# Kernel optimization log

Hardware: AMD Instinct MI355X
Metric: run time of the kernel (lower is better)

## Reference

```python
import jax, jax.numpy as jnp
import numpy as np

B, S, DIM, H = 1, 4096, 1024, 16
HEAD_DIM = DIM // H
ROPE_THETA = 10000.0
LN_EPS = 1e-5


def _rope_cos_sin(seq_len, dim, theta):
    # frequencies over the FULL model dim (rope applied before head split, as in source)
    inv_freq = 1.0 / (theta ** (jnp.arange(0, dim, 2, dtype=jnp.float32) / dim))  # (dim/2,)
    ang = jnp.arange(seq_len, dtype=jnp.float32)[:, None] * inv_freq[None, :]     # (S, dim/2)
    cos = jnp.concatenate([jnp.cos(ang), jnp.cos(ang)], axis=-1)                  # (S, dim)
    sin = jnp.concatenate([jnp.sin(ang), jnp.sin(ang)], axis=-1)
    return cos, sin


def _rotate_half(x):
    d = x.shape[-1] // 2
    return jnp.concatenate([-x[..., d:], x[..., :d]], axis=-1)


def _apply_rope(x, cos, sin):
    # x: (B, S, dim); cos/sin: (S, dim)
    return x * cos[None] + _rotate_half(x) * sin[None]


def setup_inputs() -> dict:
    key = jax.random.key(0)
    ks = jax.random.split(key, 5)
    sc = 1.0 / np.sqrt(DIM)
    return {
        "x": jax.random.normal(ks[0], (B, S, DIM), dtype=jnp.float32),
        "Wqkv": jax.random.normal(ks[1], (DIM, 3 * DIM), dtype=jnp.float32) * sc,
        "bqkv": jax.random.normal(ks[2], (3 * DIM,), dtype=jnp.float32) * 0.01,
        "Wo": jax.random.normal(ks[3], (DIM, DIM), dtype=jnp.float32) * sc,
        "bo": jax.random.normal(ks[4], (DIM,), dtype=jnp.float32) * 0.01,
        "gamma": jnp.ones((DIM,), dtype=jnp.float32),
        "beta": jnp.zeros((DIM,), dtype=jnp.float32),
    }


def reference(x, Wqkv, bqkv, Wo, bo, gamma, beta):
    b, s, d = x.shape
    qkv = x @ Wqkv + bqkv                      # (B, S, 3*dim)
    q, k, v = jnp.split(qkv, 3, axis=-1)       # each (B, S, dim)
    cos, sin = _rope_cos_sin(s, d, ROPE_THETA)
    q = _apply_rope(q, cos, sin)
    k = _apply_rope(k, cos, sin)
    # split heads
    q = q.reshape(b, s, H, HEAD_DIM)
    k = k.reshape(b, s, H, HEAD_DIM)
    v = v.reshape(b, s, H, HEAD_DIM)
    scale = 1.0 / np.sqrt(HEAD_DIM)
    scores = jnp.einsum('bqhd,bkhd->bhqk', q, k) * scale  # (B, H, S, S)
    causal = jnp.triu(jnp.ones((s, s), dtype=bool), k=1)
    scores = jnp.where(causal[None, None], -jnp.inf, scores)
    attn = jax.nn.softmax(scores, axis=-1)
    out = jnp.einsum('bhqk,bkhd->bqhd', attn, v).reshape(b, s, d)
    out = out @ Wo + bo
    # LayerNorm (dropout is identity in eval mode)
    mu = jnp.mean(out, axis=-1, keepdims=True)
    var = jnp.mean(jnp.square(out - mu), axis=-1, keepdims=True)
    return (out - mu) * jax.lax.rsqrt(var + LN_EPS) * gamma + beta
```

## Files before the change

kernel.cpp:

```cpp
#include <hip/hip_runtime.h>
#include <cstdint>
#include <cstddef>

#define S_LEN 4096
#define DIM   1024
#define NH    16
#define HD    64
#define QKV_N 3072

typedef __attribute__((ext_vector_type(8))) short short8;
typedef __attribute__((ext_vector_type(4))) float f32x4;
typedef __attribute__((ext_vector_type(4))) unsigned short ushort4v;
typedef __attribute__((ext_vector_type(2))) unsigned int uint2v;

__device__ inline unsigned short f2bf(float x) {
    unsigned int u = __builtin_bit_cast(unsigned int, x);
    u += 0x7fffu + ((u >> 16) & 1u);
    return (unsigned short)(u >> 16);
}
__device__ inline float bf2f(unsigned short u) {
    return __builtin_bit_cast(float, (unsigned int)u << 16);
}
__device__ inline unsigned int pack2_bf16_rh(float lo, float hi) {
    unsigned int a = __builtin_bit_cast(unsigned int, lo) + 0x8000u;
    unsigned int b = __builtin_bit_cast(unsigned int, hi) + 0x8000u;
    return __builtin_amdgcn_perm(b, a, 0x07060302u);
}

__device__ inline void gl_lds16(const void* g, void* l) {
    __builtin_amdgcn_global_load_lds(
        (const __attribute__((address_space(1))) void*)g,
        (__attribute__((address_space(3))) void*)l, 16, 0, 0);
}

template <bool BF16OUT>
__global__ __launch_bounds__(256) void gemm_mfma_kernel(
    const unsigned short* __restrict__ A,
    const unsigned short* __restrict__ Bt,
    const float* __restrict__ bias,
    void* __restrict__ Cv,
    int M, int N, int K)
{
    __shared__ unsigned short As[128 * 32];
    __shared__ unsigned short Bs[128 * 32];

    const int t    = threadIdx.x;
    const int w    = t >> 6;
    const int lane = t & 63;
    const int ln   = lane & 15;
    const int quad = lane >> 4;
    const int bm   = blockIdx.y * 128;
    const int bn   = blockIdx.x * 128;
    const int wm   = (w & 1) * 64;
    const int wn   = (w >> 1) * 64;

    f32x4 acc[4][4];
#pragma unroll
    for (int i = 0; i < 4; ++i)
#pragma unroll
        for (int j = 0; j < 4; ++j) acc[i][j] = (f32x4){0.f, 0.f, 0.f, 0.f};

    const int lr = lane >> 2;
    const int lc = (lane & 3) * 8;
    const unsigned short* ga = A  + (size_t)(bm + w * 32 + lr) * K + lc;
    const unsigned short* gb = Bt + (size_t)(bn + w * 32 + lr) * K + lc;
    unsigned short* la = &As[(w * 32) * 32];
    unsigned short* lb = &Bs[(w * 32) * 32];

    for (int k0 = 0; k0 < K; k0 += 32) {
        gl_lds16(ga,            la);
        gl_lds16(ga + 16 * K,   la + 16 * 32);
        gl_lds16(gb,            lb);
        gl_lds16(gb + 16 * K,   lb + 16 * 32);
        ga += 32; gb += 32;
        __syncthreads();

        short8 af[4], bf[4];
#pragma unroll
        for (int i = 0; i < 4; ++i)
            af[i] = *(const short8*)&As[(wm + i * 16 + ln) * 32 + quad * 8];
#pragma unroll
        for (int j = 0; j < 4; ++j)
            bf[j] = *(const short8*)&Bs[(wn + j * 16 + ln) * 32 + quad * 8];
#pragma unroll
        for (int i = 0; i < 4; ++i)
#pragma unroll
            for (int j = 0; j < 4; ++j)
                acc[i][j] = __builtin_amdgcn_mfma_f32_16x16x32_bf16(af[i], bf[j], acc[i][j], 0, 0, 0);
        __syncthreads();
    }

#pragma unroll
    for (int j = 0; j < 4; ++j) {
        const int col = bn + wn + j * 16 + ln;
        const float bv = bias[col];
#pragma unroll
        for (int i = 0; i < 4; ++i) {
            const int row0 = bm + wm + i * 16 + quad * 4;
#pragma unroll
            for (int r = 0; r < 4; ++r) {
                const float v = acc[i][j][r] + bv;
                if (BF16OUT)
                    ((unsigned short*)Cv)[(size_t)(row0 + r) * N + col] = f2bf(v);
                else
                    ((float*)Cv)[(size_t)(row0 + r) * N + col] = v;
            }
        }
    }
}

__global__ __launch_bounds__(256) void prep1_kernel(
    const float* __restrict__ x, unsigned short* __restrict__ xb,
    const float* __restrict__ Wqkv, unsigned short* __restrict__ WqkvT,
    const float* __restrict__ Wo, unsigned short* __restrict__ WoT)
{
    __shared__ unsigned short L[64][72];
    const int b = blockIdx.x;
    const int t = threadIdx.x;

    if (b < 2048) {
        const size_t i = ((size_t)b * 256 + t) * 8;
        float4 a = *(const float4*)(x + i);
        float4 c = *(const float4*)(x + i + 4);
        short8 p = { (short)f2bf(a.x), (short)f2bf(a.y), (short)f2bf(a.z), (short)f2bf(a.w),
                     (short)f2bf(c.x), (short)f2bf(c.y), (short)f2bf(c.z), (short)f2bf(c.w) };
        *(short8*)(xb + i) = p;
        return;
    }
    const float* W;
    unsigned short* Wt;
    int N, n0, k0;
    if (b < 2816) {
        const int wb = b - 2048;
        W = Wqkv; Wt = WqkvT; N = QKV_N;
        n0 = (wb % 48) * 64; k0 = (wb / 48) * 64;
    } else {
        const int wb = b - 2816;
        W = Wo; Wt = WoT; N = DIM;
        n0 = (wb & 15) * 64; k0 = (wb >> 4) * 64;
    }
    const int kr = t >> 2, cb = (t & 3) * 16;
    const float* wp = W + (size_t)(k0 + kr) * N + n0 + cb;
#pragma unroll
    for (int u = 0; u < 16; u += 4) {
        float4 v = *(const float4*)(wp + u);
        ushort4v p = { f2bf(v.x), f2bf(v.y), f2bf(v.z), f2bf(v.w) };
        *(ushort4v*)&L[kr][cb + u] = p;
    }
    __syncthreads();
    const int nr = t >> 2, kb = (t & 3) * 16;
    short8 lo, hi;
#pragma unroll
    for (int u = 0; u < 8; ++u) lo[u] = (short)L[kb + u][nr];
#pragma unroll
    for (int u = 0; u < 8; ++u) hi[u] = (short)L[kb + 8 + u][nr];
    unsigned short* op = Wt + (size_t)(n0 + nr) * 1024 + k0 + kb;
    *(short8*)op       = lo;
    *(short8*)(op + 8) = hi;
}

__global__ __launch_bounds__(256) void prep2_kernel(
    const unsigned short* __restrict__ qkvb,
    unsigned short* __restrict__ Qb,
    unsigned short* __restrict__ Kb,
    unsigned short* __restrict__ Vt)
{
    __shared__ unsigned short L[64][72];
    const int b = blockIdx.x;
    const int t = threadIdx.x;

    if (b < 2048) {
        const int idx = b * 256 + t;
        const int j   = (idx & 127) * 4;
        const int s   = idx >> 7;
        const unsigned short* row = qkvb + (size_t)s * QKV_N;
        unsigned short* qo = Qb + (size_t)s * DIM;
        unsigned short* ko = Kb + (size_t)s * DIM;
        const float sf = (float)s;
        const float QSCALE = 0.18033688011112042f;
        const float C1 = -0.025952563241307517f;
        const float INV2PI = 0.15915494309189535f;

        float cs[4], sn[4];
#pragma unroll
        for (int e = 0; e < 4; ++e) {
            const float invf2pi = exp2f((float)(j + e) * C1) * INV2PI;
            float rev = sf * invf2pi;
            rev -= floorf(rev);
            sn[e] = __builtin_amdgcn_sinf(rev);
            cs[e] = __builtin_amdgcn_cosf(rev);
        }
        ushort4v q1 = *(const ushort4v*)(row + j);
        ushort4v q2 = *(const ushort4v*)(row + 512 + j);
        ushort4v k1 = *(const ushort4v*)(row + DIM + j);
        ushort4v k2 = *(const ushort4v*)(row + DIM + 512 + j);
        ushort4v qa, qb4, ka, kb4;
#pragma unroll
        for (int e = 0; e < 4; ++e) {
            const float x1 = bf2f(q1[e]), x2 = bf2f(q2[e]);
            const float y1 = bf2f(k1[e]), y2 = bf2f(k2[e]);
            qa[e]  = f2bf((x1 * cs[e] - x2 * sn[e]) * QSCALE);
            qb4[e] = f2bf((x2 * cs[e] + x1 * sn[e]) * QSCALE);
            ka[e]  = f2bf(y1 * cs[e] - y2 * sn[e]);
            kb4[e] = f2bf(y2 * cs[e] + y1 * sn[e]);
        }
        *(ushort4v*)(qo + j)       = qa;
        *(ushort4v*)(qo + 512 + j) = qb4;
        *(ushort4v*)(ko + j)       = ka;
        *(ushort4v*)(ko + 512 + j) = kb4;
        return;
    }

    const int vb = b - 2048;
    const int c0 = (vb & 15) * 64;
    const int bs = (vb >> 4) * 64;
    const int sl = t >> 2, cb = (t & 3) * 16;
    const unsigned short* vp = qkvb + (size_t)(bs + sl) * QKV_N + 2 * DIM + c0 + cb;
    *(short8*)&L[sl][cb]     = *(const short8*)vp;
    *(short8*)&L[sl][cb + 8] = *(const short8*)(vp + 8);
    __syncthreads();
    const int cl = t >> 2, sb = (t & 3) * 16;
    short8 lo, hi;
#pragma unroll
    for (int u = 0; u < 8; ++u) lo[u] = (short)L[sb + u][cl];
#pragma unroll
    for (int u = 0; u < 8; ++u) hi[u] = (short)L[sb + 8 + u][cl];
    unsigned short* op = Vt + (size_t)(c0 + cl) * S_LEN + bs + sb;
    *(short8*)op       = lo;
    *(short8*)(op + 8) = hi;
}

__global__ __launch_bounds__(256) void attn_mfma_kernel(
    const unsigned short* __restrict__ Qb,
    const unsigned short* __restrict__ Kb,
    const unsigned short* __restrict__ Vt,
    float* __restrict__ Op,
    float* __restrict__ lp)
{
    __shared__ unsigned short Ks[64][72];
    __shared__ unsigned short Vs[64][72];
    __shared__ unsigned short Ps[4][16][72];

    const int t    = threadIdx.x;
    const int w    = t >> 6;
    const int lane = t & 63;
    const int ln   = lane & 15;
    const int quad = lane >> 4;
    const int p    = blockIdx.x;
    const int half = blockIdx.y;
    const int h    = blockIdx.z;

    const int sc_ = t >> 2;
    const int so  = (t & 3) * 16;

#pragma unroll
    for (int phase = 0; phase < 2; ++phase) {
        const int qt  = phase == 0 ? (63 - p) : p;
        const int q0  = qt * 64;
        const int nkt = qt + 1;
        const int c0  = (nkt + 1) >> 1;
        const int kt_begin = half == 0 ? 0 : c0;
        const int kt_end   = half == 0 ? c0 : nkt;

        short8 qf[2];
        {
            const unsigned short* qp = Qb + (size_t)(q0 + w * 16 + ln) * DIM + h * HD + quad * 8;
            qf[0] = *(const short8*)qp;
            qf[1] = *(const short8*)(qp + 32);
        }

        f32x4 o[4];
#pragma unroll
        for (int db = 0; db < 4; ++db) o[db] = (f32x4){0.f, 0.f, 0.f, 0.f};
        float lrow = 0.f;

        short8 kr0, kr1, vr0, vr1;
        {
            const int k0 = kt_begin * 64;
            const unsigned short* kp = Kb + (size_t)(k0 + sc_) * DIM + h * HD + so;
            kr0 = *(const short8*)kp;  kr1 = *(const short8*)(kp + 8);
            const unsigned short* vp = Vt + (size_t)(h * HD + sc_) * S_LEN + k0 + so;
            vr0 = *(const short8*)vp;  vr1 = *(const short8*)(vp + 8);
        }

        for (int kt = kt_begin; kt < kt_end; ++kt) {
            __syncthreads();
            *(short8*)&Ks[sc_][so]     = kr0;
            *(short8*)&Ks[sc_][so + 8] = kr1;
            *(short8*)&Vs[sc_][so]     = vr0;
            *(short8*)&Vs[sc_][so + 8] = vr1;
            if (kt + 1 < kt_end) {
                const int k1 = (kt + 1) * 64;
                const unsigned short* kp = Kb + (size_t)(k1 + sc_) * DIM + h * HD + so;
                kr0 = *(const short8*)kp;  kr1 = *(const short8*)(kp + 8);
                const unsigned short* vp = Vt + (size_t)(h * HD + sc_) * S_LEN + k1 + so;
                vr0 = *(const short8*)vp;  vr1 = *(const short8*)(vp + 8);
            }
            __syncthreads();

            f32x4 sc[4];
#pragma unroll
            for (int kb = 0; kb < 4; ++kb) sc[kb] = (f32x4){0.f, 0.f, 0.f, 0.f};
#pragma unroll
            for (int kk = 0; kk < 2; ++kk) {
#pragma unroll
                for (int kb = 0; kb < 4; ++kb) {
                    short8 kf = *(const short8*)&Ks[kb * 16 + ln][kk * 32 + quad * 8];
                    sc[kb] = __builtin_amdgcn_mfma_f32_16x16x32_bf16(kf, qf[kk], sc[kb], 0, 0, 0);
                }
            }

            if (kt == nkt - 1) {
                const int qg = w * 16 + ln;
                const int kb0 = kt * 64 - q0;
#pragma unroll
                for (int kb = 0; kb < 4; ++kb) {
                    const int key = kb0 + kb * 16 + quad * 4;
#pragma unroll
                    for (int r = 0; r < 4; ++r)
                        if (key + r > qg) sc[kb][r] = -1e30f;
                }
            }

            float psp[4];
#pragma unroll
            for (int kb = 0; kb < 4; ++kb) {
                float pv[4];
#pragma unroll
                for (int r = 0; r < 4; ++r) pv[r] = exp2f(sc[kb][r]);
                psp[kb] = (pv[0] + pv[1]) + (pv[2] + pv[3]);
                uint2v pk = { pack2_bf16_rh(pv[0], pv[1]), pack2_bf16_rh(pv[2], pv[3]) };
                *(uint2v*)&Ps[w][ln][kb * 16 + quad * 4] = pk;
            }
            float ps = (psp[0] + psp[1]) + (psp[2] + psp[3]);
            ps += __shfl_xor(ps, 16);
            ps += __shfl_xor(ps, 32);
            lrow += ps;

#pragma unroll
            for (int kk = 0; kk < 2; ++kk) {
                short8 pf = *(const short8*)&Ps[w][ln][kk * 32 + quad * 8];
#pragma unroll
                for (int db = 0; db < 4; ++db) {
                    short8 vf = *(const short8*)&Vs[db * 16 + ln][kk * 32 + quad * 8];
                    o[db] = __builtin_amdgcn_mfma_f32_16x16x32_bf16(vf, pf, o[db], 0, 0, 0);
                }
            }
        }

        {
            float* op = Op + ((size_t)half * S_LEN + q0 + w * 16 + ln) * DIM + h * HD + quad * 4;
#pragma unroll
            for (int db = 0; db < 4; ++db)
                *(f32x4*)(op + db * 16) = o[db];
            if (quad == 0)
                lp[((size_t)half * NH + h) * S_LEN + q0 + w * 16 + ln] = lrow;
        }
    }
}

__global__ __launch_bounds__(256) void combine_kernel(
    const float* __restrict__ Op, const float* __restrict__ lp,
    unsigned short* __restrict__ attnb)
{
    const int row = blockIdx.x;
    const int t   = threadIdx.x;
    const int d   = t * 4;
    const int h   = t >> 4;
    f32x4 a = *(const f32x4*)&Op[(size_t)row * DIM + d];
    f32x4 b = *(const f32x4*)&Op[((size_t)S_LEN + row) * DIM + d];
    const float l = lp[(size_t)h * S_LEN + row] + lp[((size_t)NH + h) * S_LEN + row];
    const float inv = 1.0f / l;
    ushort4v o;
#pragma unroll
    for (int e = 0; e < 4; ++e) o[e] = f2bf((a[e] + b[e]) * inv);
    *(ushort4v*)&attnb[(size_t)row * DIM + d] = o;
}

__global__ __launch_bounds__(256) void ln_kernel(
    const float* __restrict__ in, const float* __restrict__ gamma,
    const float* __restrict__ beta, float* __restrict__ out)
{
    const int row = blockIdx.x;
    const int t = threadIdx.x;
    const float4 v = *(const float4*)&in[(size_t)row * DIM + t * 4];
    float s  = v.x + v.y + v.z + v.w;
    float sq = v.x * v.x + v.y * v.y + v.z * v.z + v.w * v.w;
#pragma unroll
    for (int off = 1; off < 64; off <<= 1) {
        s  += __shfl_xor(s, off);
        sq += __shfl_xor(sq, off);
    }
    __shared__ float red[8];
    const int wv = t >> 6, ln = t & 63;
    if (ln == 0) { red[wv] = s; red[4 + wv] = sq; }
    __syncthreads();
    s  = red[0] + red[1] + red[2] + red[3];
    sq = red[4] + red[5] + red[6] + red[7];
    const float mu  = s * (1.0f / DIM);
    const float var = sq * (1.0f / DIM) - mu * mu;
    const float rs  = rsqrtf(var + 1e-5f);
    const float4 g = *(const float4*)&gamma[t * 4];
    const float4 b = *(const float4*)&beta[t * 4];
    float4 o = { (v.x - mu) * rs * g.x + b.x,
                 (v.y - mu) * rs * g.y + b.y,
                 (v.z - mu) * rs * g.z + b.z,
                 (v.w - mu) * rs * g.w + b.w };
    *(float4*)&out[(size_t)row * DIM + t * 4] = o;
}

extern "C" void kernel_launch(void* const* d_in, const int* in_sizes, int n_in,
                              void* d_out, int out_size, void* d_ws, size_t ws_size,
                              hipStream_t stream)
{
    const float* x     = (const float*)d_in[0];
    const float* Wqkv  = (const float*)d_in[1];
    const float* bqkv  = (const float*)d_in[2];
    const float* Wo    = (const float*)d_in[3];
    const float* bo    = (const float*)d_in[4];
    const float* gamma = (const float*)d_in[5];
    const float* beta  = (const float*)d_in[6];
    float* out = (float*)d_out;

    char* base = (char*)d_ws;
    unsigned short* qkvb  = (unsigned short*)base;
    unsigned short* attnb = (unsigned short*)base;
    float* Op   = (float*)(base + (size_t)8 * 1024 * 1024);
    float* proj = (float*)(base + (size_t)8 * 1024 * 1024);
    float* lp   = (float*)(base + (size_t)40 * 1024 * 1024);
    unsigned short* Qb    = (unsigned short*)(base + (size_t)48 * 1024 * 1024);
    unsigned short* Kb    = (unsigned short*)(base + (size_t)56 * 1024 * 1024);
    unsigned short* Vt    = (unsigned short*)(base + (size_t)64 * 1024 * 1024);
    unsigned short* xb    = (unsigned short*)(base + (size_t)72 * 1024 * 1024);
    unsigned short* WqkvT = (unsigned short*)(base + (size_t)80 * 1024 * 1024);
    unsigned short* WoT   = (unsigned short*)(base + (size_t)86 * 1024 * 1024);

    prep1_kernel<<<3072, 256, 0, stream>>>(x, xb, Wqkv, WqkvT, Wo, WoT);

    gemm_mfma_kernel<true><<<dim3(QKV_N / 128, S_LEN / 128), 256, 0, stream>>>(
        xb, WqkvT, bqkv, qkvb, S_LEN, QKV_N, DIM);

    prep2_kernel<<<3072, 256, 0, stream>>>(qkvb, Qb, Kb, Vt);

    attn_mfma_kernel<<<dim3(32, 2, NH), 256, 0, stream>>>(Qb, Kb, Vt, Op, lp);

    combine_kernel<<<S_LEN, 256, 0, stream>>>(Op, lp, attnb);

    gemm_mfma_kernel<false><<<dim3(DIM / 128, S_LEN / 128), 256, 0, stream>>>(
        attnb, WoT, bo, proj, S_LEN, DIM, DIM);

    ln_kernel<<<S_LEN, 256, 0, stream>>>(proj, gamma, beta, out);
}
```

Baseline: 257.2 us.

## Split attention keys across waves, keep P in registers via fp16 MFMA

Each wave now owns a 16-key slice of the 64-key tile for all 64 queries, rather than 16 queries against all keys. The softmax probabilities go straight from registers into 16x16x16 fp16 MFMAs as packed halves, with V stored transposed in fp16, so the LDS round trip for P is gone. K/V tiles are double-buffered so each iteration needs only one barrier. In exchange, partial outputs must be reduced across the four waves through LDS at the end, which costs serialized barriers and more accumulator registers. fp16 also narrows V's range compared with bf16.

```diff
diff --git a/kernel.cpp b/kernel.cpp
--- a/kernel.cpp
+++ b/kernel.cpp
@@ -12,6 +12,8 @@
 typedef __attribute__((ext_vector_type(4))) float f32x4;
 typedef __attribute__((ext_vector_type(4))) unsigned short ushort4v;
 typedef __attribute__((ext_vector_type(2))) unsigned int uint2v;
+typedef __attribute__((ext_vector_type(4))) _Float16 half4;
+typedef __attribute__((ext_vector_type(2))) _Float16 half2v;
 
 __device__ inline unsigned short f2bf(float x) {
     unsigned int u = __builtin_bit_cast(unsigned int, x);
@@ -20,11 +22,6 @@
 }
 __device__ inline float bf2f(unsigned short u) {
     return __builtin_bit_cast(float, (unsigned int)u << 16);
-}
-__device__ inline unsigned int pack2_bf16_rh(float lo, float hi) {
-    unsigned int a = __builtin_bit_cast(unsigned int, lo) + 0x8000u;
-    unsigned int b = __builtin_bit_cast(unsigned int, hi) + 0x8000u;
-    return __builtin_amdgcn_perm(b, a, 0x07060302u);
 }
 
 __device__ inline void gl_lds16(const void* g, void* l) {
@@ -222,9 +219,11 @@
     const int cl = t >> 2, sb = (t & 3) * 16;
     short8 lo, hi;
 #pragma unroll
-    for (int u = 0; u < 8; ++u) lo[u] = (short)L[sb + u][cl];
-#pragma unroll
-    for (int u = 0; u < 8; ++u) hi[u] = (short)L[sb + 8 + u][cl];
+    for (int u = 0; u < 8; ++u)
+        lo[u] = (short)__builtin_bit_cast(unsigned short, (_Float16)bf2f(L[sb + u][cl]));
+#pragma unroll
+    for (int u = 0; u < 8; ++u)
+        hi[u] = (short)__builtin_bit_cast(unsigned short, (_Float16)bf2f(L[sb + 8 + u][cl]));
     unsigned short* op = Vt + (size_t)(c0 + cl) * S_LEN + bs + sb;
     *(short8*)op       = lo;
     *(short8*)(op + 8) = hi;
@@ -237,9 +236,9 @@
     float* __restrict__ Op,
     float* __restrict__ lp)
 {
-    __shared__ unsigned short Ks[64][72];
-    __shared__ unsigned short Vs[64][72];
-    __shared__ unsigned short Ps[4][16][72];
+    __shared__ unsigned short KsM[2][64][72];
+    __shared__ unsigned short VsM[2][64][72];
+    __shared__ float lred[4][64];
 
     const int t    = threadIdx.x;
     const int w    = t >> 6;
@@ -247,115 +246,152 @@
     const int ln   = lane & 15;
     const int quad = lane >> 4;
     const int p    = blockIdx.x;
-    const int half = blockIdx.y;
+    const int hf   = blockIdx.y;
     const int h    = blockIdx.z;
 
-    const int sc_ = t >> 2;
-    const int so  = (t & 3) * 16;
-
-#pragma unroll
+    const int srow = t >> 2;
+    const int scol = (t & 3) * 16;
+
     for (int phase = 0; phase < 2; ++phase) {
         const int qt  = phase == 0 ? (63 - p) : p;
         const int q0  = qt * 64;
         const int nkt = qt + 1;
         const int c0  = (nkt + 1) >> 1;
-        const int kt_begin = half == 0 ? 0 : c0;
-        const int kt_end   = half == 0 ? c0 : nkt;
-
-        short8 qf[2];
-        {
-            const unsigned short* qp = Qb + (size_t)(q0 + w * 16 + ln) * DIM + h * HD + quad * 8;
-            qf[0] = *(const short8*)qp;
-            qf[1] = *(const short8*)(qp + 32);
-        }
-
-        f32x4 o[4];
-#pragma unroll
-        for (int db = 0; db < 4; ++db) o[db] = (f32x4){0.f, 0.f, 0.f, 0.f};
-        float lrow = 0.f;
+        const int kt_begin = hf ? c0 : 0;
+        const int kt_end   = hf ? nkt : c0;
+
+        short8 qf[4][2];
+#pragma unroll
+        for (int qb = 0; qb < 4; ++qb) {
+            const unsigned short* qp = Qb + (size_t)(q0 + qb * 16 + ln) * DIM + h * HD + quad * 8;
+            qf[qb][0] = *(const short8*)qp;
+            qf[qb][1] = *(const short8*)(qp + 32);
+        }
+
+        f32x4 o[4][4];
+#pragma unroll
+        for (int db = 0; db < 4; ++db)
+#pragma unroll
+            for (int qb = 0; qb < 4; ++qb) o[db][qb] = (f32x4){0.f, 0.f, 0.f, 0.f};
+        float lac[4] = {0.f, 0.f, 0.f, 0.f};
 
         short8 kr0, kr1, vr0, vr1;
         {
             const int k0 = kt_begin * 64;
-            const unsigned short* kp = Kb + (size_t)(k0 + sc_) * DIM + h * HD + so;
-            kr0 = *(const short8*)kp;  kr1 = *(const short8*)(kp + 8);
-            const unsigned short* vp = Vt + (size_t)(h * HD + sc_) * S_LEN + k0 + so;
-            vr0 = *(const short8*)vp;  vr1 = *(const short8*)(vp + 8);
-        }
+            const unsigned short* kp = Kb + (size_t)(k0 + srow) * DIM + h * HD + scol;
+            kr0 = *(const short8*)kp;       kr1 = *(const short8*)(kp + 8);
+            const unsigned short* vp = Vt + (size_t)(h * HD + srow) * S_LEN + k0 + scol;
+            vr0 = *(const short8*)vp;       vr1 = *(const short8*)(vp + 8);
+        }
+        int cur = 0;
+        *(short8*)&KsM[0][srow][scol]     = kr0;
+        *(short8*)&KsM[0][srow][scol + 8] = kr1;
+        *(short8*)&VsM[0][srow][scol]     = vr0;
+        *(short8*)&VsM[0][srow][scol + 8] = vr1;
+        __syncthreads();
 
         for (int kt = kt_begin; kt < kt_end; ++kt) {
+            const bool more = (kt + 1 < kt_end);
+            if (more) {
+                const int k1 = (kt + 1) * 64;
+                const unsigned short* kp = Kb + (size_t)(k1 + srow) * DIM + h * HD + scol;
+                kr0 = *(const short8*)kp;   kr1 = *(const short8*)(kp + 8);
+                const unsigned short* vp = Vt + (size_t)(h * HD + srow) * S_LEN + k1 + scol;
+                vr0 = *(const short8*)vp;   vr1 = *(const short8*)(vp + 8);
+            }
+
+            f32x4 sc[4];
+#pragma unroll
+            for (int qb = 0; qb < 4; ++qb) sc[qb] = (f32x4){0.f, 0.f, 0.f, 0.f};
+#pragma unroll
+            for (int kk = 0; kk < 2; ++kk) {
+                short8 kf = *(const short8*)&KsM[cur][w * 16 + ln][kk * 32 + quad * 8];
+#pragma unroll
+                for (int qb = 0; qb < 4; ++qb)
+                    sc[qb] = __builtin_amdgcn_mfma_f32_16x16x32_bf16(kf, qf[qb][kk], sc[qb], 0, 0, 0);
+            }
+
+            if (kt == nkt - 1) {
+                const int keyb = kt * 64 + w * 16 + quad * 4;
+#pragma unroll
+                for (int qb = 0; qb < 4; ++qb) {
+                    const int qg = q0 + qb * 16 + ln;
+#pragma unroll
+                    for (int r = 0; r < 4; ++r)
+                        if (keyb + r > qg) sc[qb][r] = -1e30f;
+                }
+            }
+
+            half4 pf[4];
+#pragma unroll
+            for (int qb = 0; qb < 4; ++qb) {
+                const float p0 = exp2f(sc[qb][0]);
+                const float p1 = exp2f(sc[qb][1]);
+                const float p2 = exp2f(sc[qb][2]);
+                const float p3 = exp2f(sc[qb][3]);
+                lac[qb] += (p0 + p1) + (p2 + p3);
+                half2v lo2 = __builtin_bit_cast(half2v, __builtin_amdgcn_cvt_pkrtz(p0, p1));
+                half2v hi2 = __builtin_bit_cast(half2v, __builtin_amdgcn_cvt_pkrtz(p2, p3));
+                pf[qb] = (half4){lo2[0], lo2[1], hi2[0], hi2[1]};
+            }
+
+#pragma unroll
+            for (int db = 0; db < 4; ++db) {
+                half4 vf = *(const half4*)&VsM[cur][db * 16 + ln][w * 16 + quad * 4];
+#pragma unroll
+                for (int qb = 0; qb < 4; ++qb)
+                    o[db][qb] = __builtin_amdgcn_mfma_f32_16x16x16f16(vf, pf[qb], o[db][qb], 0, 0, 0);
+            }
+
+            if (more) {
+                cur ^= 1;
+                *(short8*)&KsM[cur][srow][scol]     = kr0;
+                *(short8*)&KsM[cur][srow][scol + 8] = kr1;
+                *(short8*)&VsM[cur][srow][scol]     = vr0;
+                *(short8*)&VsM[cur][srow][scol + 8] = vr1;
+            }
             __syncthreads();
-            *(short8*)&Ks[sc_][so]     = kr0;
-            *(short8*)&Ks[sc_][so + 8] = kr1;
-            *(short8*)&Vs[sc_][so]     = vr0;
-            *(short8*)&Vs[sc_][so + 8] = vr1;
-            if (kt + 1 < kt_end) {
-                const int k1 = (kt + 1) * 64;
-                const unsigned short* kp = Kb + (size_t)(k1 + sc_) * DIM + h * HD + so;
-                kr0 = *(const short8*)kp;  kr1 = *(const short8*)(kp + 8);
-                const unsigned short* vp = Vt + (size_t)(h * HD + sc_) * S_LEN + k1 + so;
-                vr0 = *(const short8*)vp;  vr1 = *(const short8*)(vp + 8);
+        }
+
+#pragma unroll
+        for (int qb = 0; qb < 4; ++qb) {
+            lac[qb] += __shfl_xor(lac[qb], 16);
+            lac[qb] += __shfl_xor(lac[qb], 32);
+        }
+        if (quad == 0) {
+#pragma unroll
+            for (int qb = 0; qb < 4; ++qb) lred[w][qb * 16 + ln] = lac[qb];
+        }
+
+        float* Ored = (float*)&KsM[0][0][0];
+        __syncthreads();
+        for (int wv = 0; wv < 4; ++wv) {
+            if (w == wv) {
+#pragma unroll
+                for (int db = 0; db < 4; ++db)
+#pragma unroll
+                    for (int qb = 0; qb < 4; ++qb) {
+                        float* ad = &Ored[(qb * 16 + ln) * 72 + db * 16 + quad * 4];
+                        f32x4 v = o[db][qb];
+                        if (wv != 0) v += *(const f32x4*)ad;
+                        *(f32x4*)ad = v;
+                    }
             }
             __syncthreads();
-
-            f32x4 sc[4];
-#pragma unroll
-            for (int kb = 0; kb < 4; ++kb) sc[kb] = (f32x4){0.f, 0.f, 0.f, 0.f};
-#pragma unroll
-            for (int kk = 0; kk < 2; ++kk) {
-#pragma unroll
-                for (int kb = 0; kb < 4; ++kb) {
-                    short8 kf = *(const short8*)&Ks[kb * 16 + ln][kk * 32 + quad * 8];
-                    sc[kb] = __builtin_amdgcn_mfma_f32_16x16x32_bf16(kf, qf[kk], sc[kb], 0, 0, 0);
-                }
-            }
-
-            if (kt == nkt - 1) {
-                const int qg = w * 16 + ln;
-                const int kb0 = kt * 64 - q0;
-#pragma unroll
-                for (int kb = 0; kb < 4; ++kb) {
-                    const int key = kb0 + kb * 16 + quad * 4;
-#pragma unroll
-                    for (int r = 0; r < 4; ++r)
-                        if (key + r > qg) sc[kb][r] = -1e30f;
-                }
-            }
-
-            float psp[4];
-#pragma unroll
-            for (int kb = 0; kb < 4; ++kb) {
-                float pv[4];
-#pragma unroll
-                for (int r = 0; r < 4; ++r) pv[r] = exp2f(sc[kb][r]);
-                psp[kb] = (pv[0] + pv[1]) + (pv[2] + pv[3]);
-                uint2v pk = { pack2_bf16_rh(pv[0], pv[1]), pack2_bf16_rh(pv[2], pv[3]) };
-                *(uint2v*)&Ps[w][ln][kb * 16 + quad * 4] = pk;
-            }
-            float ps = (psp[0] + psp[1]) + (psp[2] + psp[3]);
-            ps += __shfl_xor(ps, 16);
-            ps += __shfl_xor(ps, 32);
-            lrow += ps;
-
-#pragma unroll
-            for (int kk = 0; kk < 2; ++kk) {
-                short8 pf = *(const short8*)&Ps[w][ln][kk * 32 + quad * 8];
-#pragma unroll
-                for (int db = 0; db < 4; ++db) {
-                    short8 vf = *(const short8*)&Vs[db * 16 + ln][kk * 32 + quad * 8];
-                    o[db] = __builtin_amdgcn_mfma_f32_16x16x32_bf16(vf, pf, o[db], 0, 0, 0);
-                }
-            }
         }
 
         {
-            float* op = Op + ((size_t)half * S_LEN + q0 + w * 16 + ln) * DIM + h * HD + quad * 4;
-#pragma unroll
-            for (int db = 0; db < 4; ++db)
-                *(f32x4*)(op + db * 16) = o[db];
-            if (quad == 0)
-                lp[((size_t)half * NH + h) * S_LEN + q0 + w * 16 + ln] = lrow;
-        }
+            const int q  = t >> 2;
+            const int d0 = (t & 3) * 16;
+            float* op = Op + ((size_t)hf * S_LEN + q0 + q) * DIM + h * HD + d0;
+#pragma unroll
+            for (int c = 0; c < 4; ++c)
+                *(f32x4*)(op + c * 4) = *(const f32x4*)&Ored[q * 72 + d0 + c * 4];
+            if (t < 64)
+                lp[((size_t)hf * NH + h) * S_LEN + q0 + t] =
+                    lred[0][t] + lred[1][t] + lred[2][t] + lred[3][t];
+        }
+        __syncthreads();
     }
 }
 
```

Result: slower. 270.1 us (+5.0%).

## Split attention keys four ways and keep probabilities in registers via fp16 MFMA

Applied to the files above, without the earlier changes.

The attention kernel now splits each query tile's key range into four chunks instead of two, doubling the grid to expose more parallelism. Partial outputs are stored as bf16 instead of fp32, and the combine kernel sums four partials. The P·V product now uses the 16x16x16 fp16 MFMA with probabilities packed straight from registers, which removes the per-wave LDS round trip for P. V is converted to fp16 during transposition. The trade-offs are more partial-output traffic and extra combine work, plus reduced precision from bf16 partials and truncating fp16 conversion of the probabilities.

```diff
diff --git a/kernel.cpp b/kernel.cpp
--- a/kernel.cpp
+++ b/kernel.cpp
@@ -7,11 +7,14 @@
 #define NH    16
 #define HD    64
 #define QKV_N 3072
+#define NSPLIT 4
 
 typedef __attribute__((ext_vector_type(8))) short short8;
 typedef __attribute__((ext_vector_type(4))) float f32x4;
 typedef __attribute__((ext_vector_type(4))) unsigned short ushort4v;
 typedef __attribute__((ext_vector_type(2))) unsigned int uint2v;
+typedef __attribute__((ext_vector_type(4))) _Float16 half4;
+typedef __attribute__((ext_vector_type(2))) _Float16 half2v;
 
 __device__ inline unsigned short f2bf(float x) {
     unsigned int u = __builtin_bit_cast(unsigned int, x);
@@ -222,9 +225,11 @@
     const int cl = t >> 2, sb = (t & 3) * 16;
     short8 lo, hi;
 #pragma unroll
-    for (int u = 0; u < 8; ++u) lo[u] = (short)L[sb + u][cl];
-#pragma unroll
-    for (int u = 0; u < 8; ++u) hi[u] = (short)L[sb + 8 + u][cl];
+    for (int u = 0; u < 8; ++u)
+        lo[u] = (short)__builtin_bit_cast(unsigned short, (_Float16)bf2f(L[sb + u][cl]));
+#pragma unroll
+    for (int u = 0; u < 8; ++u)
+        hi[u] = (short)__builtin_bit_cast(unsigned short, (_Float16)bf2f(L[sb + 8 + u][cl]));
     unsigned short* op = Vt + (size_t)(c0 + cl) * S_LEN + bs + sb;
     *(short8*)op       = lo;
     *(short8*)(op + 8) = hi;
@@ -234,12 +239,11 @@
     const unsigned short* __restrict__ Qb,
     const unsigned short* __restrict__ Kb,
     const unsigned short* __restrict__ Vt,
-    float* __restrict__ Op,
+    unsigned short* __restrict__ Opb,
     float* __restrict__ lp)
 {
     __shared__ unsigned short Ks[64][72];
     __shared__ unsigned short Vs[64][72];
-    __shared__ unsigned short Ps[4][16][72];
 
     const int t    = threadIdx.x;
     const int w    = t >> 6;
@@ -247,20 +251,18 @@
     const int ln   = lane & 15;
     const int quad = lane >> 4;
     const int p    = blockIdx.x;
-    const int half = blockIdx.y;
+    const int hf   = blockIdx.y;
     const int h    = blockIdx.z;
 
-    const int sc_ = t >> 2;
-    const int so  = (t & 3) * 16;
-
-#pragma unroll
+    const int srow = t >> 2;
+    const int scol = (t & 3) * 16;
+
     for (int phase = 0; phase < 2; ++phase) {
         const int qt  = phase == 0 ? (63 - p) : p;
         const int q0  = qt * 64;
         const int nkt = qt + 1;
-        const int c0  = (nkt + 1) >> 1;
-        const int kt_begin = half == 0 ? 0 : c0;
-        const int kt_end   = half == 0 ? c0 : nkt;
+        const int kt_begin = (nkt * hf) >> 2;
+        const int kt_end   = (nkt * (hf + 1)) >> 2;
 
         short8 qf[2];
         {
@@ -272,29 +274,29 @@
         f32x4 o[4];
 #pragma unroll
         for (int db = 0; db < 4; ++db) o[db] = (f32x4){0.f, 0.f, 0.f, 0.f};
-        float lrow = 0.f;
+        float lac = 0.f;
 
         short8 kr0, kr1, vr0, vr1;
         {
             const int k0 = kt_begin * 64;
-            const unsigned short* kp = Kb + (size_t)(k0 + sc_) * DIM + h * HD + so;
-            kr0 = *(const short8*)kp;  kr1 = *(const short8*)(kp + 8);
-            const unsigned short* vp = Vt + (size_t)(h * HD + sc_) * S_LEN + k0 + so;
-            vr0 = *(const short8*)vp;  vr1 = *(const short8*)(vp + 8);
+            const unsigned short* kp = Kb + (size_t)(k0 + srow) * DIM + h * HD + scol;
+            kr0 = *(const short8*)kp;       kr1 = *(const short8*)(kp + 8);
+            const unsigned short* vp = Vt + (size_t)(h * HD + srow) * S_LEN + k0 + scol;
+            vr0 = *(const short8*)vp;       vr1 = *(const short8*)(vp + 8);
         }
 
         for (int kt = kt_begin; kt < kt_end; ++kt) {
             __syncthreads();
-            *(short8*)&Ks[sc_][so]     = kr0;
-            *(short8*)&Ks[sc_][so + 8] = kr1;
-            *(short8*)&Vs[sc_][so]     = vr0;
-            *(short8*)&Vs[sc_][so + 8] = vr1;
+            *(short8*)&Ks[srow][scol]     = kr0;
+            *(short8*)&Ks[srow][scol + 8] = kr1;
+            *(short8*)&Vs[srow][scol]     = vr0;
+            *(short8*)&Vs[srow][scol + 8] = vr1;
             if (kt + 1 < kt_end) {
                 const int k1 = (kt + 1) * 64;
-                const unsigned short* kp = Kb + (size_t)(k1 + sc_) * DIM + h * HD + so;
-                kr0 = *(const short8*)kp;  kr1 = *(const short8*)(kp + 8);
-                const unsigned short* vp = Vt + (size_t)(h * HD + sc_) * S_LEN + k1 + so;
-                vr0 = *(const short8*)vp;  vr1 = *(const short8*)(vp + 8);
+                const unsigned short* kp = Kb + (size_t)(k1 + srow) * DIM + h * HD + scol;
+                kr0 = *(const short8*)kp;   kr1 = *(const short8*)(kp + 8);
+                const unsigned short* vp = Vt + (size_t)(h * HD + srow) * S_LEN + k1 + scol;
+                vr0 = *(const short8*)vp;   vr1 = *(const short8*)(vp + 8);
             }
             __syncthreads();
 
@@ -311,69 +313,76 @@
             }
 
             if (kt == nkt - 1) {
-                const int qg = w * 16 + ln;
-                const int kb0 = kt * 64 - q0;
+                const int qg = q0 + w * 16 + ln;
 #pragma unroll
                 for (int kb = 0; kb < 4; ++kb) {
-                    const int key = kb0 + kb * 16 + quad * 4;
+                    const int key = kt * 64 + kb * 16 + quad * 4;
 #pragma unroll
                     for (int r = 0; r < 4; ++r)
                         if (key + r > qg) sc[kb][r] = -1e30f;
                 }
             }
 
-            float psp[4];
+            half4 pf[4];
 #pragma unroll
             for (int kb = 0; kb < 4; ++kb) {
-                float pv[4];
-#pragma unroll
-                for (int r = 0; r < 4; ++r) pv[r] = exp2f(sc[kb][r]);
-                psp[kb] = (pv[0] + pv[1]) + (pv[2] + pv[3]);
-                uint2v pk = { pack2_bf16_rh(pv[0], pv[1]), pack2_bf16_rh(pv[2], pv[3]) };
-                *(uint2v*)&Ps[w][ln][kb * 16 + quad * 4] = pk;
-            }
-            float ps = (psp[0] + psp[1]) + (psp[2] + psp[3]);
-            ps += __shfl_xor(ps, 16);
-            ps += __shfl_xor(ps, 32);
-            lrow += ps;
-
-#pragma unroll
-            for (int kk = 0; kk < 2; ++kk) {
-                short8 pf = *(const short8*)&Ps[w][ln][kk * 32 + quad * 8];
-#pragma unroll
-                for (int db = 0; db < 4; ++db) {
-                    short8 vf = *(const short8*)&Vs[db * 16 + ln][kk * 32 + quad * 8];
-                    o[db] = __builtin_amdgcn_mfma_f32_16x16x32_bf16(vf, pf, o[db], 0, 0, 0);
+                const float p0 = exp2f(sc[kb][0]);
+                const float p1 = exp2f(sc[kb][1]);
+                const float p2 = exp2f(sc[kb][2]);
+                const float p3 = exp2f(sc[kb][3]);
+                lac += (p0 + p1) + (p2 + p3);
+                half2v lo2 = __builtin_bit_cast(half2v, __builtin_amdgcn_cvt_pkrtz(p0, p1));
+                half2v hi2 = __builtin_bit_cast(half2v, __builtin_amdgcn_cvt_pkrtz(p2, p3));
+                pf[kb] = (half4){lo2[0], lo2[1], hi2[0], hi2[1]};
+            }
+
+#pragma unroll
+            for (int db = 0; db < 4; ++db) {
+#pragma unroll
+                for (int kb = 0; kb < 4; ++kb) {
+                    half4 vf = *(const half4*)&Vs[db * 16 + ln][kb * 16 + quad * 4];
+                    o[db] = __builtin_amdgcn_mfma_f32_16x16x16f16(vf, pf[kb], o[db], 0, 0, 0);
                 }
             }
         }
 
-        {
-            float* op = Op + ((size_t)half * S_LEN + q0 + w * 16 + ln) * DIM + h * HD + quad * 4;
-#pragma unroll
-            for (int db = 0; db < 4; ++db)
-                *(f32x4*)(op + db * 16) = o[db];
-            if (quad == 0)
-                lp[((size_t)half * NH + h) * S_LEN + q0 + w * 16 + ln] = lrow;
-        }
+        lac += __shfl_xor(lac, 16);
+        lac += __shfl_xor(lac, 32);
+
+        unsigned short* op = Opb + ((size_t)hf * S_LEN + q0 + w * 16 + ln) * DIM
+                                 + h * HD + quad * 4;
+#pragma unroll
+        for (int db = 0; db < 4; ++db) {
+            uint2v pk = { pack2_bf16_rh(o[db][0], o[db][1]),
+                          pack2_bf16_rh(o[db][2], o[db][3]) };
+            *(uint2v*)(op + db * 16) = pk;
+        }
+        if (quad == 0)
+            lp[((size_t)hf * NH + h) * S_LEN + q0 + w * 16 + ln] = lac;
     }
 }
 
 __global__ __launch_bounds__(256) void combine_kernel(
-    const float* __restrict__ Op, const float* __restrict__ lp,
+    const unsigned short* __restrict__ Opb, const float* __restrict__ lp,
     unsigned short* __restrict__ attnb)
 {
     const int row = blockIdx.x;
     const int t   = threadIdx.x;
     const int d   = t * 4;
     const int h   = t >> 4;
-    f32x4 a = *(const f32x4*)&Op[(size_t)row * DIM + d];
-    f32x4 b = *(const f32x4*)&Op[((size_t)S_LEN + row) * DIM + d];
-    const float l = lp[(size_t)h * S_LEN + row] + lp[((size_t)NH + h) * S_LEN + row];
+    f32x4 acc = (f32x4){0.f, 0.f, 0.f, 0.f};
+    float l = 0.f;
+#pragma unroll
+    for (int i = 0; i < NSPLIT; ++i) {
+        ushort4v a = *(const ushort4v*)&Opb[((size_t)i * S_LEN + row) * DIM + d];
+#pragma unroll
+        for (int e = 0; e < 4; ++e) acc[e] += bf2f(a[e]);
+        l += lp[((size_t)i * NH + h) * S_LEN + row];
+    }
     const float inv = 1.0f / l;
     ushort4v o;
 #pragma unroll
-    for (int e = 0; e < 4; ++e) o[e] = f2bf((a[e] + b[e]) * inv);
+    for (int e = 0; e < 4; ++e) o[e] = f2bf(acc[e] * inv);
     *(ushort4v*)&attnb[(size_t)row * DIM + d] = o;
 }
 
@@ -425,7 +434,7 @@
     char* base = (char*)d_ws;
     unsigned short* qkvb  = (unsigned short*)base;
     unsigned short* attnb = (unsigned short*)base;
-    float* Op   = (float*)(base + (size_t)8 * 1024 * 1024);
+    unsigned short* Opb   = (unsigned short*)(base + (size_t)8 * 1024 * 1024);
     float* proj = (float*)(base + (size_t)8 * 1024 * 1024);
     float* lp   = (float*)(base + (size_t)40 * 1024 * 1024);
     unsigned short* Qb    = (unsigned short*)(base + (size_t)48 * 1024 * 1024);
@@ -442,9 +451,9 @@
 
     prep2_kernel<<<3072, 256, 0, stream>>>(qkvb, Qb, Kb, Vt);
 
-    attn_mfma_kernel<<<dim3(32, 2, NH), 256, 0, stream>>>(Qb, Kb, Vt, Op, lp);
-
-    combine_kernel<<<S_LEN, 256, 0, stream>>>(Op, lp, attnb);
+    attn_mfma_kernel<<<dim3(32, NSPLIT, NH), 256, 0, stream>>>(Qb, Kb, Vt, Opb, lp);
+
+    combine_kernel<<<S_LEN, 256, 0, stream>>>(Opb, lp, attnb);
 
     gemm_mfma_kernel<false><<<dim3(DIM / 128, S_LEN / 128), 256, 0, stream>>>(
         attnb, WoT, bo, proj, S_LEN, DIM, DIM);
```

After: 257.7 us. About the same (+0.2%).
